# Kernel optimization log

Measured on AMD Instinct MI355X. Metric: run time of the kernel, lower is better.

The kernel has to match this reference:

```python
import jax, jax.numpy as jnp
import numpy as np

NUM_NODES = 1024
NUM_HEADS = 8
HIDDEN = 256
BOND_DIM = 64
NUM_LAYERS = 3


def _build_edge_index(n):
    # ring + chord graph, both directions -> 4n directed edges, no duplicate (src,tgt) pairs
    u = np.arange(n)
    src = np.concatenate([u, u, (u + 1) % n, (u + 2) % n])
    dst = np.concatenate([(u + 1) % n, (u + 2) % n, u, u])
    return jnp.asarray(np.stack([src, dst]), dtype=jnp.int32)


def setup_inputs() -> dict:
    key = jax.random.key(0)
    ks = jax.random.split(key, 16)
    H, L, B = HIDDEN, NUM_LAYERS, BOND_DIM
    E = 4 * NUM_NODES
    s = 0.02
    inp = {
        "edge_index": _build_edge_index(NUM_NODES),
        "bond_features": jax.random.normal(ks[0], (E, B), jnp.float32),
        # bond_embedding Linear + W_h Linear (stored as [in, out])
        "W_emb": jax.random.normal(ks[1], (B, H), jnp.float32) * s,
        "b_emb": jnp.zeros((H,), jnp.float32),
        "W_h": jax.random.normal(ks[2], (H, H), jnp.float32) * s,
        "b_h": jnp.zeros((H,), jnp.float32),
        # per-layer attention block: pre-LN, qkv in-proj, out-proj
        "ln1_g": jnp.ones((L, H), jnp.float32),
        "ln1_b": jnp.zeros((L, H), jnp.float32),
        "in_w": jax.random.normal(ks[3], (L, H, 3 * H), jnp.float32) * s,
        "in_b": jnp.zeros((L, 3 * H), jnp.float32),
        "out_w": jax.random.normal(ks[4], (L, H, H), jnp.float32) * s,
        "out_b": jnp.zeros((L, H), jnp.float32),
        # per-layer bond_update: Linear -> LayerNorm -> GELU
        "up_w": jax.random.normal(ks[5], (L, H, H), jnp.float32) * s,
        "up_b": jnp.zeros((L, H), jnp.float32),
        "ln2_g": jnp.ones((L, H), jnp.float32),
        "ln2_b": jnp.zeros((L, H), jnp.float32),
    }
    return inp


def _layer_norm(x, g, b, eps=1e-5):
    m = jnp.mean(x, axis=-1, keepdims=True)
    v = jnp.var(x, axis=-1, keepdims=True)
    return (x - m) * jax.lax.rsqrt(v + eps) * g + b


def _mha(x, in_w, in_b, out_w, out_b):
    # x: [E, H]; standard torch MultiheadAttention (batch of 1)
    E, H = x.shape
    d = H // NUM_HEADS
    qkv = x @ in_w + in_b                                  # [E, 3H]
    q, k, v = jnp.split(qkv, 3, axis=-1)
    q = q.reshape(E, NUM_HEADS, d).transpose(1, 0, 2)       # [h, E, d]
    k = k.reshape(E, NUM_HEADS, d).transpose(1, 0, 2)
    v = v.reshape(E, NUM_HEADS, d).transpose(1, 0, 2)
    scores = jnp.einsum("hqd,hkd->hqk", q, k) / jnp.sqrt(jnp.float32(d))
    p = jax.nn.softmax(scores, axis=-1)
    o = jnp.einsum("hqk,hkd->hqd", p, v)                    # [h, E, d]
    o = o.transpose(1, 0, 2).reshape(E, H)
    return o @ out_w + out_b


def _bond_aggregation(edge_index, h):
    # r_e = sum_{e' : tgt(e')=tgt(e), src(e')!=src(e)} (h[e'] - h[e])
    # with no duplicate (src,tgt) pairs this is S[tgt] - deg[tgt] * h
    tgt = edge_index[1]
    S = jax.ops.segment_sum(h, tgt, num_segments=NUM_NODES)                 # [N, H]
    deg = jax.ops.segment_sum(jnp.ones(h.shape[:1], h.dtype), tgt, num_segments=NUM_NODES)
    return S[tgt] - deg[tgt][:, None] * h


def reference(edge_index, bond_features, W_emb, b_emb, W_h, b_h,
              ln1_g, ln1_b, in_w, in_b, out_w, out_b,
              up_w, up_b, ln2_g, ln2_b):
    h = jax.nn.gelu(bond_features @ W_emb + b_emb, approximate=False)
    h = h @ W_h + b_h
    for t in range(NUM_LAYERS):
        r = _bond_aggregation(edge_index, h)
        xn = _layer_norm(r, ln1_g[t], ln1_b[t])
        attn = _mha(xn, in_w[t], in_b[t], out_w[t], out_b[t])
        # block output = attn + r (residual inside block), forward adds + r again
        t_ij = attn + r + r
        u = t_ij @ up_w[t] + up_b[t]
        h = jax.nn.gelu(_layer_norm(u, ln2_g[t], ln2_b[t]), approximate=False)
    return h
```

## Files before the change

### kernel.cpp

```cpp
#include <hip/hip_runtime.h>
#include <hip/hip_bf16.h>
#include <math.h>

#define N_NODES 1024
#define NE      4096
#define HDIM    256
#define QSCALE  0.2550348634f

typedef __hip_bfloat16 bf16;
typedef __attribute__((ext_vector_type(8))) short bf16x8;
typedef __attribute__((ext_vector_type(4))) float f32x4;

__device__ __forceinline__ float u2f(unsigned short u) {
  return __uint_as_float(((unsigned)u) << 16);
}
__device__ __forceinline__ short f2bs(float x) {
  unsigned u = __float_as_uint(x);
  unsigned r = u + 0x7FFFu + ((u >> 16) & 1u);
  return (short)(r >> 16);
}
__device__ __forceinline__ float gelu_f(float x) {
  return 0.5f * x * (1.0f + erff(x * 0.70710678118654752f));
}
__device__ __forceinline__ short rdbf(const void* p, int i, int flag) {
  return flag ? ((const short*)p)[i] : f2bs(((const float*)p)[i]);
}
__device__ __forceinline__ float fexp2(float x) {
#if __has_builtin(__builtin_amdgcn_exp2f)
  return __builtin_amdgcn_exp2f(x);
#else
  return exp2f(x);
#endif
}
__device__ __forceinline__ unsigned pk2(float lo, float hi) {
  return (__float_as_uint(hi) & 0xFFFF0000u) | (__float_as_uint(lo) >> 16);
}

__global__ __launch_bounds__(64) void k_detect(const unsigned* __restrict__ w,
                                               int* __restrict__ flag) {
  int t = threadIdx.x;
  int cnt = 0;
  for (int i = 0; i < 16; ++i) {
    unsigned v = w[t * 16 + i];
    unsigned e = (v >> 7) & 0xFFu;
    cnt += (e >= 100u && e <= 132u) ? 1 : 0;
  }
#pragma unroll
  for (int k = 1; k < 64; k <<= 1) cnt += __shfl_xor(cnt, k, 64);
  if (t == 0) *flag = (cnt > 512) ? 1 : 0;
}

struct WPtrs { const void* w_emb; const void* w_h; const void* in_w;
               const void* out_w; const void* up_w; };
__global__ __launch_bounds__(256) void k_prep_w(WPtrs a, short* __restrict__ Wt,
                                                const int* __restrict__ flag) {
  int i = blockIdx.x * 256 + threadIdx.x;
  if (i >= 1064960) return;
  const int fl = *flag;
  if (i < 16384) {
    int k = i >> 8, n = i & 255;
    Wt[n * 64 + k] = rdbf(a.w_emb, i, fl);
  } else if (i < 81920) {
    int j = i - 16384;
    int k = j >> 8, n = j & 255;
    Wt[16384 + n * 256 + k] = rdbf(a.w_h, j, fl);
  } else if (i < 671744) {
    int j = i - 81920;
    int t = j / 196608, jj = j % 196608;
    int k = jj / 768, n = jj % 768;
    Wt[81920 + t * 196608 + n * 256 + k] = rdbf(a.in_w, j, fl);
  } else if (i < 868352) {
    int j = i - 671744;
    int t = j >> 16, jj = j & 65535;
    int k = jj >> 8, n = jj & 255;
    Wt[671744 + t * 65536 + n * 256 + k] = rdbf(a.out_w, j, fl);
  } else {
    int j = i - 868352;
    int t = j >> 16, jj = j & 65535;
    int k = jj >> 8, n = jj & 255;
    Wt[868352 + t * 65536 + n * 256 + k] = rdbf(a.up_w, j, fl);
  }
}

struct PPtrs { const void* p[9]; };
__global__ __launch_bounds__(256) void k_cvt_small(PPtrs a, float* __restrict__ dst,
                                                   const int* __restrict__ flag) {
  const int sz[9] = {256, 256, 768, 768, 2304, 768, 768, 768, 768};
  int i = blockIdx.x * 256 + threadIdx.x;
  if (i >= 7424) return;
  int seg = 0, off = i;
  while (off >= sz[seg]) { off -= sz[seg]; ++seg; }
  dst[i] = *flag ? u2f(((const unsigned short*)a.p[seg])[off])
                 : ((const float*)a.p[seg])[off];
}

__global__ __launch_bounds__(256) void k_cvt_bond(const void* __restrict__ src,
                                                  short* __restrict__ dst,
                                                  const int* __restrict__ flag) {
  int i = blockIdx.x * 256 + threadIdx.x;
  if (i < NE * 64) dst[i] = rdbf(src, i, *flag);
}

__global__ __launch_bounds__(256) void k_build_inv(const int* __restrict__ tgt,
                                                   int* __restrict__ cnt,
                                                   int* __restrict__ inv) {
  int e = blockIdx.x * 256 + threadIdx.x;
  if (e < NE) {
    int t = tgt[e];
    int s = atomicAdd(&cnt[t], 1);
    if (s < 8) inv[t * 8 + s] = e;
  }
}

template <bool GELU, bool RES, bool WF, bool WB>
__global__ __launch_bounds__(256) void k_mgemm(const short* __restrict__ A,
                                               const short* __restrict__ Bt,
                                               const float* __restrict__ bias,
                                               const float* __restrict__ res,
                                               float* __restrict__ outF,
                                               short* __restrict__ outB,
                                               int M, int N, int K) {
  __shared__ alignas(16) short As[64 * 40];
  __shared__ alignas(16) short Bs[64 * 40];
  const int tid = threadIdx.x;
  const int wave = tid >> 6, lane = tid & 63;
  const int m = lane & 15, quad = lane >> 4;
  const int bm = blockIdx.x * 64, bn = blockIdx.y * 64;
  const int m0 = (wave & 1) * 32, n0 = (wave >> 1) * 32;
  const int srow = tid >> 2, sko = (tid & 3) * 8;

  f32x4 acc[2][2];
  acc[0][0] = acc[0][1] = acc[1][0] = acc[1][1] = (f32x4){0.f, 0.f, 0.f, 0.f};

  int4 pa = *(const int4*)(A + (size_t)(bm + srow) * K + sko);
  int4 pb = *(const int4*)(Bt + (size_t)(bn + srow) * K + sko);

  for (int k0 = 0; k0 < K; k0 += 32) {
    __syncthreads();
    *(int4*)&As[srow * 40 + sko] = pa;
    *(int4*)&Bs[srow * 40 + sko] = pb;
    __syncthreads();
    if (k0 + 32 < K) {
      pa = *(const int4*)(A + (size_t)(bm + srow) * K + k0 + 32 + sko);
      pb = *(const int4*)(Bt + (size_t)(bn + srow) * K + k0 + 32 + sko);
    }
    bf16x8 a0 = *(const bf16x8*)&As[(m0 + m) * 40 + quad * 8];
    bf16x8 a1 = *(const bf16x8*)&As[(m0 + 16 + m) * 40 + quad * 8];
    bf16x8 b0 = *(const bf16x8*)&Bs[(n0 + m) * 40 + quad * 8];
    bf16x8 b1 = *(const bf16x8*)&Bs[(n0 + 16 + m) * 40 + quad * 8];
    acc[0][0] = __builtin_amdgcn_mfma_f32_16x16x32_bf16(a0, b0, acc[0][0], 0, 0, 0);
    acc[0][1] = __builtin_amdgcn_mfma_f32_16x16x32_bf16(a0, b1, acc[0][1], 0, 0, 0);
    acc[1][0] = __builtin_amdgcn_mfma_f32_16x16x32_bf16(a1, b0, acc[1][0], 0, 0, 0);
    acc[1][1] = __builtin_amdgcn_mfma_f32_16x16x32_bf16(a1, b1, acc[1][1], 0, 0, 0);
  }

#pragma unroll
  for (int i = 0; i < 2; ++i)
#pragma unroll
    for (int j = 0; j < 2; ++j) {
      const int col = bn + n0 + j * 16 + m;
      const float bv = bias[col];
#pragma unroll
      for (int r = 0; r < 4; ++r) {
        const int row = bm + m0 + i * 16 + quad * 4 + r;
        float v = acc[i][j][r] + bv;
        if (GELU) v = gelu_f(v);
        if (RES) v += 2.0f * res[(size_t)row * N + col];
        if (WF) outF[(size_t)row * N + col] = v;
        if (WB) outB[(size_t)row * N + col] = f2bs(v);
      }
    }
}

__global__ __launch_bounds__(256) void k_mgemm_qkv(const short* __restrict__ A,
                                                   const short* __restrict__ Bt,
                                                   const float* __restrict__ bias,
                                                   short* __restrict__ Qh,
                                                   short* __restrict__ Kh,
                                                   short* __restrict__ Vt) {
  const int K = 256;
  __shared__ alignas(16) short As[64 * 40];
  __shared__ alignas(16) short Bs[64 * 40];
  const int tid = threadIdx.x;
  const int wave = tid >> 6, lane = tid & 63;
  const int m = lane & 15, quad = lane >> 4;
  const int bm = blockIdx.x * 64, bn = blockIdx.y * 64;
  const int m0 = (wave & 1) * 32, n0 = (wave >> 1) * 32;
  const int srow = tid >> 2, sko = (tid & 3) * 8;

  f32x4 acc[2][2];
  acc[0][0] = acc[0][1] = acc[1][0] = acc[1][1] = (f32x4){0.f, 0.f, 0.f, 0.f};

  int4 pa = *(const int4*)(A + (size_t)(bm + srow) * K + sko);
  int4 pb = *(const int4*)(Bt + (size_t)(bn + srow) * K + sko);

  for (int k0 = 0; k0 < K; k0 += 32) {
    __syncthreads();
    *(int4*)&As[srow * 40 + sko] = pa;
    *(int4*)&Bs[srow * 40 + sko] = pb;
    __syncthreads();
    if (k0 + 32 < K) {
      pa = *(const int4*)(A + (size_t)(bm + srow) * K + k0 + 32 + sko);
      pb = *(const int4*)(Bt + (size_t)(bn + srow) * K + k0 + 32 + sko);
    }
    bf16x8 a0 = *(const bf16x8*)&As[(m0 + m) * 40 + quad * 8];
    bf16x8 a1 = *(const bf16x8*)&As[(m0 + 16 + m) * 40 + quad * 8];
    bf16x8 b0 = *(const bf16x8*)&Bs[(n0 + m) * 40 + quad * 8];
    bf16x8 b1 = *(const bf16x8*)&Bs[(n0 + 16 + m) * 40 + quad * 8];
    acc[0][0] = __builtin_amdgcn_mfma_f32_16x16x32_bf16(a0, b0, acc[0][0], 0, 0, 0);
    acc[0][1] = __builtin_amdgcn_mfma_f32_16x16x32_bf16(a0, b1, acc[0][1], 0, 0, 0);
    acc[1][0] = __builtin_amdgcn_mfma_f32_16x16x32_bf16(a1, b0, acc[1][0], 0, 0, 0);
    acc[1][1] = __builtin_amdgcn_mfma_f32_16x16x32_bf16(a1, b1, acc[1][1], 0, 0, 0);
  }

#pragma unroll
  for (int i = 0; i < 2; ++i)
#pragma unroll
    for (int j = 0; j < 2; ++j) {
      const int col = bn + n0 + j * 16 + m;
      const float bv = bias[col];
      const int row0 = bm + m0 + i * 16 + quad * 4;
      if (col < 256) {
        const int head = col >> 5, d = col & 31;
#pragma unroll
        for (int r = 0; r < 4; ++r)
          Qh[(size_t)head * 131072 + (row0 + r) * 32 + d] =
              f2bs((acc[i][j][r] + bv) * QSCALE);
      } else if (col < 512) {
        const int c = col - 256, head = c >> 5, d = c & 31;
#pragma unroll
        for (int r = 0; r < 4; ++r)
          Kh[(size_t)head * 131072 + (row0 + r) * 32 + d] = f2bs(acc[i][j][r] + bv);
      } else {
        const int c = col - 512, head = c >> 5, d = c & 31;
        const int p0 = (row0 & ~63) + ((row0 >> 5) & 1) * 32 +
                       ((row0 >> 2) & 3) * 8 + ((row0 >> 4) & 1) * 4;
        ushort4 w;
        w.x = (unsigned short)f2bs(acc[i][j][0] + bv);
        w.y = (unsigned short)f2bs(acc[i][j][1] + bv);
        w.z = (unsigned short)f2bs(acc[i][j][2] + bv);
        w.w = (unsigned short)f2bs(acc[i][j][3] + bv);
        *(ushort4*)(Vt + (size_t)head * 131072 + d * 4096 + p0) = w;
      }
    }
}

__global__ __launch_bounds__(256) void k_rln2(const int* __restrict__ tgt,
                                              const int* __restrict__ cnt,
                                              const int* __restrict__ inv,
                                              const float* __restrict__ h,
                                              const float* __restrict__ g,
                                              const float* __restrict__ b,
                                              float* __restrict__ r,
                                              short* __restrict__ xnb) {
  __shared__ float red1[4], red2[4];
  const int e = blockIdx.x, d = threadIdx.x;
  const int t = tgt[e];
  const int c = cnt[t];
  float S = 0.f;
  for (int j = 0; j < c; ++j)
    S += h[(size_t)inv[t * 8 + j] * HDIM + d];
  float rv = S - (float)c * h[(size_t)e * HDIM + d];
  r[(size_t)e * HDIM + d] = rv;

  float s = rv;
#pragma unroll
  for (int k = 1; k < 64; k <<= 1) s += __shfl_xor(s, k, 64);
  if ((d & 63) == 0) red1[d >> 6] = s;
  __syncthreads();
  float mean = (red1[0] + red1[1] + red1[2] + red1[3]) * (1.0f / HDIM);
  float diff = rv - mean;
  float sq = diff * diff;
#pragma unroll
  for (int k = 1; k < 64; k <<= 1) sq += __shfl_xor(sq, k, 64);
  if ((d & 63) == 0) red2[d >> 6] = sq;
  __syncthreads();
  float var = (red2[0] + red2[1] + red2[2] + red2[3]) * (1.0f / HDIM);
  xnb[(size_t)e * HDIM + d] = f2bs(diff * rsqrtf(var + 1e-5f) * g[d] + b[d]);
}

__global__ __launch_bounds__(256) void k_ln_gelu(const float* __restrict__ u,
                                                 const float* __restrict__ g,
                                                 const float* __restrict__ b,
                                                 float* __restrict__ hout,
                                                 void* __restrict__ finalout,
                                                 const int* __restrict__ flag) {
  __shared__ float red1[4], red2[4];
  const int e = blockIdx.x, d = threadIdx.x;
  float v = u[(size_t)e * HDIM + d];
  float s = v;
#pragma unroll
  for (int k = 1; k < 64; k <<= 1) s += __shfl_xor(s, k, 64);
  if ((d & 63) == 0) red1[d >> 6] = s;
  __syncthreads();
  float mean = (red1[0] + red1[1] + red1[2] + red1[3]) * (1.0f / HDIM);
  float diff = v - mean;
  float sq = diff * diff;
#pragma unroll
  for (int k = 1; k < 64; k <<= 1) sq += __shfl_xor(sq, k, 64);
  if ((d & 63) == 0) red2[d >> 6] = sq;
  __syncthreads();
  float var = (red2[0] + red2[1] + red2[2] + red2[3]) * (1.0f / HDIM);
  float xh = diff * rsqrtf(var + 1e-5f) * g[d] + b[d];
  float out = gelu_f(xh);
  hout[(size_t)e * HDIM + d] = out;
  if (finalout) {
    if (*flag)
      ((bf16*)finalout)[(size_t)e * HDIM + d] = __float2bfloat16(out);
    else
      ((float*)finalout)[(size_t)e * HDIM + d] = out;
  }
}

__global__ __launch_bounds__(256) void k_flash4(const short* __restrict__ Qh,
                                                const short* __restrict__ Kh,
                                                const short* __restrict__ Vt,
                                                short* __restrict__ Opart,
                                                float* __restrict__ lpart) {
  const int head = blockIdx.y, split = blockIdx.z;
  const int tid = threadIdx.x;
  const int wave = tid >> 6, lane = tid & 63;
  const int m = lane & 15, quad = lane >> 4;
  const int q0 = blockIdx.x * 256 + wave * 64;

  const short* Qb = Qh + (size_t)head * 131072;
  const short* Kb = Kh + (size_t)head * 131072;
  const short* Vb = Vt + (size_t)head * 131072;

  bf16x8 qf[4];
#pragma unroll
  for (int a = 0; a < 4; ++a)
    qf[a] = *(const bf16x8*)(Qb + (q0 + a * 16 + m) * 32 + quad * 8);

  f32x4 O[4][2];
  f32x4 lacc[4];
#pragma unroll
  for (int a = 0; a < 4; ++a) {
    O[a][0] = O[a][1] = (f32x4){0.f, 0.f, 0.f, 0.f};
    lacc[a] = (f32x4){0.f, 0.f, 0.f, 0.f};
  }

  bf16x8 ones;
#pragma unroll
  for (int i = 0; i < 8; ++i) ones[i] = (short)0x3F80;

  const int base = split * 1024;
  const short* kp = Kb + (size_t)(base + m) * 32 + quad * 8;
  const short* vp = Vb + (size_t)m * 4096 + base + quad * 8;

  bf16x8 kc0 = *(const bf16x8*)(kp);
  bf16x8 kc1 = *(const bf16x8*)(kp + 512);
  bf16x8 kc2 = *(const bf16x8*)(kp + 1024);
  bf16x8 kc3 = *(const bf16x8*)(kp + 1536);

#pragma unroll 1
  for (int kb = 0; kb < 16; ++kb) {
    const short* vq = vp + kb * 64;
    bf16x8 vc0 = *(const bf16x8*)(vq);
    bf16x8 vc1 = *(const bf16x8*)(vq + 65536);
    bf16x8 vc2 = *(const bf16x8*)(vq + 32);
    bf16x8 vc3 = *(const bf16x8*)(vq + 65536 + 32);
    const int nxt = (kb < 15) ? (kb + 1) * 2048 : 0;
    bf16x8 kn0 = *(const bf16x8*)(kp + nxt);
    bf16x8 kn1 = *(const bf16x8*)(kp + nxt + 512);
    bf16x8 kn2 = *(const bf16x8*)(kp + nxt + 1024);
    bf16x8 kn3 = *(const bf16x8*)(kp + nxt + 1536);

    const f32x4 z = {0.f, 0.f, 0.f, 0.f};
#pragma unroll
    for (int a = 0; a < 4; ++a) {
      f32x4 S0 = __builtin_amdgcn_mfma_f32_16x16x32_bf16(kc0, qf[a], z, 0, 0, 0);
      f32x4 S1 = __builtin_amdgcn_mfma_f32_16x16x32_bf16(kc1, qf[a], z, 0, 0, 0);
      f32x4 S2 = __builtin_amdgcn_mfma_f32_16x16x32_bf16(kc2, qf[a], z, 0, 0, 0);
      f32x4 S3 = __builtin_amdgcn_mfma_f32_16x16x32_bf16(kc3, qf[a], z, 0, 0, 0);

      float e0[4], e1[4], e2[4], e3[4];
#pragma unroll
      for (int r = 0; r < 4; ++r) {
        e0[r] = fexp2(S0[r]);
        e1[r] = fexp2(S1[r]);
        e2[r] = fexp2(S2[r]);
        e3[r] = fexp2(S3[r]);
      }
      union { bf16x8 v; unsigned u[4]; } pf0, pf1;
      pf0.u[0] = pk2(e0[0], e0[1]);
      pf0.u[1] = pk2(e0[2], e0[3]);
      pf0.u[2] = pk2(e1[0], e1[1]);
      pf0.u[3] = pk2(e1[2], e1[3]);
      pf1.u[0] = pk2(e2[0], e2[1]);
      pf1.u[1] = pk2(e2[2], e2[3]);
      pf1.u[2] = pk2(e3[0], e3[1]);
      pf1.u[3] = pk2(e3[2], e3[3]);

      O[a][0] = __builtin_amdgcn_mfma_f32_16x16x32_bf16(pf0.v, vc0, O[a][0], 0, 0, 0);
      O[a][1] = __builtin_amdgcn_mfma_f32_16x16x32_bf16(pf0.v, vc1, O[a][1], 0, 0, 0);
      lacc[a] = __builtin_amdgcn_mfma_f32_16x16x32_bf16(pf0.v, ones, lacc[a], 0, 0, 0);
      O[a][0] = __builtin_amdgcn_mfma_f32_16x16x32_bf16(pf1.v, vc2, O[a][0], 0, 0, 0);
      O[a][1] = __builtin_amdgcn_mfma_f32_16x16x32_bf16(pf1.v, vc3, O[a][1], 0, 0, 0);
      lacc[a] = __builtin_amdgcn_mfma_f32_16x16x32_bf16(pf1.v, ones, lacc[a], 0, 0, 0);
    }
    kc0 = kn0; kc1 = kn1; kc2 = kn2; kc3 = kn3;
  }

#pragma unroll
  for (int a = 0; a < 4; ++a)
#pragma unroll
    for (int r = 0; r < 4; ++r) {
      const int row = q0 + a * 16 + quad * 4 + r;
      short* op = Opart + ((size_t)split * 4096 + row) * 256 + head * 32 + m;
      op[0]  = f2bs(O[a][0][r]);
      op[16] = f2bs(O[a][1][r]);
      if (m == 0) lpart[(size_t)(split * 8 + head) * 4096 + row] = lacc[a][r];
    }
}

__global__ __launch_bounds__(256) void k_merge(const short* __restrict__ Opart,
                                               const float* __restrict__ lpart,
                                               short* __restrict__ attnb) {
  const int i = blockIdx.x * 256 + threadIdx.x;
  const int q = i >> 8, hd = i & 255, head = hd >> 5;
  float o = 0.f, l = 0.f;
#pragma unroll
  for (int s = 0; s < 4; ++s) {
    o += u2f((unsigned short)Opart[(size_t)s * 1048576 + i]);
    l += lpart[(size_t)(s * 8 + head) * 4096 + q];
  }
  attnb[i] = f2bs(o / l);
}

extern "C" void kernel_launch(void* const* d_in, const int* in_sizes, int n_in,
                              void* d_out, int out_size, void* d_ws, size_t ws_size,
                              hipStream_t stream) {
  const int* edge = (const int*)d_in[0];
  const int* tgt = edge + NE;

  float* ws = (float*)d_ws;
  float* hbuf   = ws;
  float* rbuf   = ws + 1048576;
  int* cnt      = (int*)(ws + 2097152);
  int* inv      = cnt + 1024;
  float* prm    = ws + 2360320;
  short* xn_bf  = (short*)(ws + 2367744);
  short* attnbf = (short*)(ws + 2892032);
  short* Wt     = (short*)(ws + 3416320);
  short* Qh     = (short*)(ws + 3948800);
  short* Kh     = (short*)(ws + 4473088);
  short* Vt     = (short*)(ws + 4997376);
  float* lpart  = ws + 5521664;
  float* BIG    = ws + 5652736;
  int* flag     = (int*)(ws + 9847040);

  short* bond_bf = (short*)BIG;
  short* e1_bf   = (short*)(BIG + 131072);
  short* Opart   = (short*)BIG;
  short* t_bf    = (short*)BIG;
  float* ubuf    = BIG + 524288;

  const short* Wt_emb = Wt;
  const short* Wt_h   = Wt + 16384;
  const short* Wt_in  = Wt + 81920;
  const short* Wt_out = Wt + 671744;
  const short* Wt_up  = Wt + 868352;
  const float* b_emb = prm;
  const float* b_h   = prm + 256;
  const float* ln1_g = prm + 512;
  const float* ln1_b = prm + 1280;
  const float* in_b  = prm + 2048;
  const float* out_b = prm + 4352;
  const float* up_b  = prm + 5120;
  const float* ln2_g = prm + 5888;
  const float* ln2_b = prm + 6656;

  k_detect<<<dim3(1), dim3(64), 0, stream>>>((const unsigned*)d_in[2], flag);
  WPtrs wp = {d_in[2], d_in[4], d_in[8], d_in[10], d_in[12]};
  k_prep_w<<<dim3(4160), dim3(256), 0, stream>>>(wp, Wt, flag);
  PPtrs pp = {{d_in[3], d_in[5], d_in[6], d_in[7], d_in[9], d_in[11],
               d_in[13], d_in[14], d_in[15]}};
  k_cvt_small<<<dim3(29), dim3(256), 0, stream>>>(pp, prm, flag);
  k_cvt_bond<<<dim3(1024), dim3(256), 0, stream>>>(d_in[1], bond_bf, flag);
  hipMemsetAsync(cnt, 0, N_NODES * sizeof(int), stream);
  k_build_inv<<<dim3(16), dim3(256), 0, stream>>>(tgt, cnt, inv);

  dim3 blk(256);
  dim3 g256(64, 4);
  dim3 g768(64, 12);
  dim3 gfa(16, 8, 4);

  k_mgemm<true, false, false, true><<<g256, blk, 0, stream>>>(
      bond_bf, Wt_emb, b_emb, nullptr, nullptr, e1_bf, NE, 256, 64);
  k_mgemm<false, false, true, false><<<g256, blk, 0, stream>>>(
      e1_bf, Wt_h, b_h, nullptr, hbuf, nullptr, NE, 256, 256);

  for (int t = 0; t < 3; ++t) {
    k_rln2<<<dim3(NE), blk, 0, stream>>>(tgt, cnt, inv, hbuf,
                                         ln1_g + t * HDIM, ln1_b + t * HDIM,
                                         rbuf, xn_bf);
    k_mgemm_qkv<<<g768, blk, 0, stream>>>(xn_bf, Wt_in + (size_t)t * 196608,
                                          in_b + t * 768, Qh, Kh, Vt);
    k_flash4<<<gfa, blk, 0, stream>>>(Qh, Kh, Vt, Opart, lpart);
    k_merge<<<dim3(4096), blk, 0, stream>>>(Opart, lpart, attnbf);
    k_mgemm<false, true, false, true><<<g256, blk, 0, stream>>>(
        attnbf, Wt_out + (size_t)t * 65536, out_b + t * 256, rbuf,
        nullptr, t_bf, NE, 256, 256);
    k_mgemm<false, false, true, false><<<g256, blk, 0, stream>>>(
        t_bf, Wt_up + (size_t)t * 65536, up_b + t * 256, nullptr,
        ubuf, nullptr, NE, 256, 256);
    k_ln_gelu<<<dim3(NE), blk, 0, stream>>>(ubuf, ln2_g + t * HDIM,
                                            ln2_b + t * HDIM, hbuf,
                                            (t == 2) ? d_out : nullptr, flag);
  }
}
```

Before: 317.4 us.

## Stage K/V tiles cooperatively in LDS for flash attention kernel

Previously each of the four waves in a block loaded its own copy of every K and V tile straight from global memory. Now all 256 threads load each K/V tile once into padded shared-memory buffers, and the next tile is prefetched into registers while the current one is used. The goal is to cut redundant global/L2 traffic and load instructions per wave. The cost is two block-wide barriers per key block and LDS reads. The V buffer uses a 70-element row stride, so its 16-byte accesses are not naturally aligned.

```diff
diff --git a/kernel.cpp b/kernel.cpp
--- a/kernel.cpp
+++ b/kernel.cpp
@@ -317,6 +317,8 @@
                                                 const short* __restrict__ Vt,
                                                 short* __restrict__ Opart,
                                                 float* __restrict__ lpart) {
+  __shared__ alignas(16) short Ks[64 * 40];
+  __shared__ alignas(16) short Vs[32 * 70 + 8];
   const int head = blockIdx.y, split = blockIdx.z;
   const int tid = threadIdx.x;
   const int wave = tid >> 6, lane = tid & 63;
@@ -345,26 +347,33 @@
   for (int i = 0; i < 8; ++i) ones[i] = (short)0x3F80;
 
   const int base = split * 1024;
-  const short* kp = Kb + (size_t)(base + m) * 32 + quad * 8;
-  const short* vp = Vb + (size_t)m * 4096 + base + quad * 8;
-
-  bf16x8 kc0 = *(const bf16x8*)(kp);
-  bf16x8 kc1 = *(const bf16x8*)(kp + 512);
-  bf16x8 kc2 = *(const bf16x8*)(kp + 1024);
-  bf16x8 kc3 = *(const bf16x8*)(kp + 1536);
+  const int krow = tid >> 2, ko = (tid & 3) * 8;
+  const int vrow = tid >> 3, vo = (tid & 7) * 8;
+  const short* kstage = Kb + (size_t)(base + krow) * 32 + ko;
+  const short* vstage = Vb + (size_t)vrow * 4096 + base + vo;
+
+  int4 rk = *(const int4*)(kstage);
+  int4 rv = *(const int4*)(vstage);
 
 #pragma unroll 1
   for (int kb = 0; kb < 16; ++kb) {
-    const short* vq = vp + kb * 64;
-    bf16x8 vc0 = *(const bf16x8*)(vq);
-    bf16x8 vc1 = *(const bf16x8*)(vq + 65536);
-    bf16x8 vc2 = *(const bf16x8*)(vq + 32);
-    bf16x8 vc3 = *(const bf16x8*)(vq + 65536 + 32);
-    const int nxt = (kb < 15) ? (kb + 1) * 2048 : 0;
-    bf16x8 kn0 = *(const bf16x8*)(kp + nxt);
-    bf16x8 kn1 = *(const bf16x8*)(kp + nxt + 512);
-    bf16x8 kn2 = *(const bf16x8*)(kp + nxt + 1024);
-    bf16x8 kn3 = *(const bf16x8*)(kp + nxt + 1536);
+    __syncthreads();
+    *(int4*)&Ks[krow * 40 + ko] = rk;
+    *(int4*)&Vs[vrow * 70 + vo] = rv;
+    __syncthreads();
+    if (kb < 15) {
+      rk = *(const int4*)(kstage + (kb + 1) * 2048);
+      rv = *(const int4*)(vstage + (kb + 1) * 64);
+    }
+
+    bf16x8 kc0 = *(const bf16x8*)&Ks[(0 * 16 + m) * 40 + quad * 8];
+    bf16x8 kc1 = *(const bf16x8*)&Ks[(1 * 16 + m) * 40 + quad * 8];
+    bf16x8 kc2 = *(const bf16x8*)&Ks[(2 * 16 + m) * 40 + quad * 8];
+    bf16x8 kc3 = *(const bf16x8*)&Ks[(3 * 16 + m) * 40 + quad * 8];
+    bf16x8 vc0 = *(const bf16x8*)&Vs[m * 70 + quad * 8];
+    bf16x8 vc1 = *(const bf16x8*)&Vs[(m + 16) * 70 + quad * 8];
+    bf16x8 vc2 = *(const bf16x8*)&Vs[m * 70 + 32 + quad * 8];
+    bf16x8 vc3 = *(const bf16x8*)&Vs[(m + 16) * 70 + 32 + quad * 8];
 
     const f32x4 z = {0.f, 0.f, 0.f, 0.f};
 #pragma unroll
@@ -399,7 +408,6 @@
       O[a][1] = __builtin_amdgcn_mfma_f32_16x16x32_bf16(pf1.v, vc3, O[a][1], 0, 0, 0);
       lacc[a] = __builtin_amdgcn_mfma_f32_16x16x32_bf16(pf1.v, ones, lacc[a], 0, 0, 0);
     }
-    kc0 = kn0; kc1 = kn1; kc2 = kn2; kc3 = kn3;
   }
 
 #pragma unroll
```

Result: no change. 312.2 us (-1.6%).
